# Performance work log

Measured on AMD Instinct MI355X. Metric: run time of the kernel, lower is better.

The kernel has to match this reference:

```python
import math
import jax, jax.numpy as jnp
import numpy as np

D, NH, NL, NP = 256, 8, 3, 4
HD = D // NH
SHAPES = np.array([[92, 92], [46, 46], [23, 23]], dtype=np.int32)
LSI = np.concatenate([[0], np.cumsum(SHAPES[:, 0] * SHAPES[:, 1])[:-1]]).astype(np.int32)
LV = int((SHAPES[:, 0] * SHAPES[:, 1]).sum())  # 11109
B, LQ = 2, LV


def setup_inputs() -> dict:
    key = jax.random.key(0)
    ks = jax.random.split(key, 8)
    query = jax.random.normal(ks[0], (B, LQ, D), jnp.float32)
    reference_points = jax.random.uniform(ks[1], (B, LQ, NL, 2), dtype=jnp.float32)
    value_flat = jax.random.normal(ks[2], (B, LV, D), jnp.float32)
    # sampling_offsets: small random weight + structured directional bias (as in _reset_parameters)
    W_off = jax.random.normal(ks[3], (D, NH * NL * NP * 2), jnp.float32) * 0.01
    thetas = np.arange(NH, dtype=np.float64) * (2.0 * math.pi / NH)
    g = np.stack([np.cos(thetas), np.sin(thetas)], axis=-1)
    g = g / np.abs(g).max(axis=-1, keepdims=True)
    g = np.tile(g[:, None, None, :], (1, NL, NP, 1))
    g = g * (np.arange(NP) + 1)[None, None, :, None]
    b_off = jnp.asarray(g.reshape(-1), jnp.float32)
    W_attn = jax.random.normal(ks[4], (D, NH * NL * NP), jnp.float32) * 0.01
    b_attn = jnp.zeros((NH * NL * NP,), jnp.float32)
    W_val = jax.random.normal(ks[5], (D, D), jnp.float32) * (1.0 / math.sqrt(D))
    b_val = jnp.zeros((D,), jnp.float32)
    W_out = jax.random.normal(ks[6], (D, D), jnp.float32) * (1.0 / math.sqrt(D))
    b_out = jnp.zeros((D,), jnp.float32)
    return dict(query=query, reference_points=reference_points, value_flat=value_flat,
                W_val=W_val, b_val=b_val, W_off=W_off, b_off=b_off,
                W_attn=W_attn, b_attn=b_attn, W_out=W_out, b_out=b_out,
                spatial_shapes=jnp.asarray(SHAPES), level_start_index=jnp.asarray(LSI))


def _bilinear_sample(val_l, grid):
    """torch.F.grid_sample(mode='bilinear', padding_mode='zeros', align_corners=False).
    val_l: [B,H,W,nH,hd]; grid: [B,Q,nH,P,2] with (x,y) in [-1,1].
    Returns [B,nH,Q,P,hd]."""
    Bq, H, W, nH, hd = val_l.shape
    Q, P = grid.shape[1], grid.shape[3]
    x = ((grid[..., 0] + 1.0) * W - 1.0) * 0.5   # pixel coords, align_corners=False
    y = ((grid[..., 1] + 1.0) * H - 1.0) * 0.5
    x0f, y0f = jnp.floor(x), jnp.floor(y)
    lx, ly = x - x0f, y - y0f
    x0, y0 = x0f.astype(jnp.int32), y0f.astype(jnp.int32)
    val_bh = val_l.transpose(0, 3, 1, 2, 4).reshape(Bq * nH, H * W, hd)

    def corner(yi, xi, w):
        valid = (xi >= 0) & (xi < W) & (yi >= 0) & (yi < H)
        idx = jnp.clip(yi, 0, H - 1) * W + jnp.clip(xi, 0, W - 1)   # [B,Q,nH,P]
        idx_bh = idx.transpose(0, 2, 1, 3).reshape(Bq * nH, Q * P)
        g = jnp.take_along_axis(val_bh, idx_bh[:, :, None], axis=1)  # [B*nH, Q*P, hd]
        wm = (w * valid.astype(w.dtype)).transpose(0, 2, 1, 3).reshape(Bq * nH, Q * P, 1)
        return g * wm

    out = (corner(y0, x0, (1 - ly) * (1 - lx)) + corner(y0, x0 + 1, (1 - ly) * lx)
           + corner(y0 + 1, x0, ly * (1 - lx)) + corner(y0 + 1, x0 + 1, ly * lx))
    return out.reshape(Bq, nH, Q, P, hd)


def reference(query, reference_points, value_flat, W_val, b_val, W_off, b_off,
              W_attn, b_attn, W_out, b_out, spatial_shapes, level_start_index):
    shapes = np.asarray(spatial_shapes)          # static level geometry
    starts = np.asarray(level_start_index)
    Bq, Lq, _ = query.shape
    value = (value_flat @ W_val + b_val).reshape(Bq, -1, NH, HD)
    off = (query @ W_off + b_off).reshape(Bq, Lq, NH, NL, NP, 2)        # (dy,dx) pixels
    aw = jax.nn.softmax((query @ W_attn + b_attn).reshape(Bq, Lq, NH, NL * NP), axis=-1)
    aw = aw.reshape(Bq, Lq, NH, NL, NP)
    sh_f = jnp.asarray(shapes, jnp.float32)                              # [L,2] = (H,W)
    norm_off = off / sh_f[None, None, None, :, None, :]
    loc = reference_points[:, :, None, :, None, :] + norm_off           # [B,Lq,NH,NL,NP,2] (y,x)
    grid = 2.0 * loc[..., ::-1] - 1.0                                    # (x,y) in [-1,1]
    out = jnp.zeros((Bq, Lq, NH, HD), query.dtype)
    for l in range(NL):
        H, W = int(shapes[l, 0]), int(shapes[l, 1])
        s = int(starts[l])
        val_l = value[:, s:s + H * W].reshape(Bq, H, W, NH, HD)
        sampled = _bilinear_sample(val_l, grid[:, :, :, l])              # [B,NH,Lq,NP,HD]
        out = out + jnp.einsum('bhqpc,bqhp->bqhc', sampled, aw[:, :, :, l])
    return out.reshape(Bq, Lq, D) @ W_out + b_out
```

## Files before the change

### kernel.cpp

```cpp
#include <hip/hip_runtime.h>

#define LQn   11109
#define MTOT  22218

typedef __attribute__((ext_vector_type(8))) short short8;
typedef __attribute__((ext_vector_type(4))) float f32x4;

__device__ __forceinline__ unsigned short f2bf(float f) {
  union { float f; unsigned int u; } v; v.f = f;
  unsigned int r = v.u + 0x7fffu + ((v.u >> 16) & 1u);
  return (unsigned short)(r >> 16);
}

__global__ __launch_bounds__(256) void prep_weights(
    const float* __restrict__ Wval, const float* __restrict__ Woff,
    const float* __restrict__ Wattn, const float* __restrict__ Wout,
    const float* __restrict__ boff, const float* __restrict__ battn,
    unsigned short* __restrict__ Wval_t, unsigned short* __restrict__ Wcat_t,
    unsigned short* __restrict__ Wout_t, float* __restrict__ bcat) {
  int i = blockIdx.x * 256 + threadIdx.x;
  int n = i >> 8, k = i & 255;
  if (n < 256) {
    Wval_t[i] = f2bf(Wval[k * 256 + n]);
    Wout_t[i] = f2bf(Wout[k * 256 + n]);
  }
  float src = (n < 192) ? Woff[k * 192 + n] : Wattn[k * 96 + (n - 192)];
  Wcat_t[i] = f2bf(src);
  if (i < 288) bcat[i] = (i < 192) ? boff[i] : battn[i - 192];
}

__global__ __launch_bounds__(256) void gemm_fused12(
    const float* __restrict__ Aval,
    const float* __restrict__ Aq,
    const unsigned short* __restrict__ Bval,
    const unsigned short* __restrict__ Bcat,
    const float* __restrict__ bval, const float* __restrict__ bcat,
    unsigned short* __restrict__ value16,
    float* __restrict__ logits) {
  __shared__ unsigned short As[8][64][40];
  __shared__ unsigned short Bs[64][40];

  const bool is2 = blockIdx.y == 1;
  const float* __restrict__ A = is2 ? Aq : Aval;
  const unsigned short* __restrict__ Bt = is2 ? Bcat : Bval;
  const float* __restrict__ bias = is2 ? bcat : bval;
  const int N = is2 ? 288 : 256;
  const int NB = is2 ? 5 : 4;

  const int bm = blockIdx.x;
  const int t = threadIdx.x;
  const int wave = t >> 6, lane = t & 63;
  const int wm = wave >> 1, wn = wave & 1;
  const int quad = lane >> 4, l16 = lane & 15;

  const int ldr = t >> 2;
  const int ldk = (t & 3) * 8;
  const int arow = bm * 64 + ldr;

  for (int kb = 0; kb < 8; kb++) {
    float4 a0 = {0.f, 0.f, 0.f, 0.f}, a1 = a0;
    if (arow < MTOT) {
      a0 = *(const float4*)(A + (size_t)arow * 256 + kb * 32 + ldk);
      a1 = *(const float4*)(A + (size_t)arow * 256 + kb * 32 + ldk + 4);
    }
    ushort4 lo, hi;
    lo.x = f2bf(a0.x); lo.y = f2bf(a0.y); lo.z = f2bf(a0.z); lo.w = f2bf(a0.w);
    hi.x = f2bf(a1.x); hi.y = f2bf(a1.y); hi.z = f2bf(a1.z); hi.w = f2bf(a1.w);
    *(ushort4*)(&As[kb][ldr][ldk]) = lo;
    *(ushort4*)(&As[kb][ldr][ldk + 4]) = hi;
  }

  for (int bn = 0; bn < NB; bn++) {
    const int brow = bn * 64 + ldr;
    f32x4 acc[2][2];
    for (int i = 0; i < 2; i++)
      for (int j = 0; j < 2; j++) acc[i][j] = (f32x4){0.f, 0.f, 0.f, 0.f};

    for (int kb = 0; kb < 8; kb++) {
      uint4 bv = {0u, 0u, 0u, 0u};
      if (brow < N) bv = *(const uint4*)(Bt + (size_t)brow * 256 + kb * 32 + ldk);
      __syncthreads();
      *(uint4*)(&Bs[ldr][ldk]) = bv;
      __syncthreads();
      short8 af[2], bfr[2];
      for (int i = 0; i < 2; i++)
        af[i] = *(const short8*)(&As[kb][wm * 32 + i * 16 + l16][quad * 8]);
      for (int j = 0; j < 2; j++)
        bfr[j] = *(const short8*)(&Bs[wn * 32 + j * 16 + l16][quad * 8]);
      for (int i = 0; i < 2; i++)
        for (int j = 0; j < 2; j++)
          acc[i][j] = __builtin_amdgcn_mfma_f32_16x16x32_bf16(af[i], bfr[j], acc[i][j], 0, 0, 0);
    }

    for (int i = 0; i < 2; i++)
      for (int j = 0; j < 2; j++) {
        int colg = bn * 64 + wn * 32 + j * 16 + l16;
        if (colg >= N) continue;
        float bsv = bias[colg];
        int row0 = bm * 64 + wm * 32 + i * 16 + quad * 4;
        for (int r = 0; r < 4; r++) {
          int rg = row0 + r;
          if (rg >= MTOT) continue;
          float v = acc[i][j][r] + bsv;
          if (is2) {
            logits[(size_t)rg * 288 + colg] = v;
          } else {
            int b = (rg >= LQn) ? 1 : 0;
            int p = rg - b * LQn;
            value16[((size_t)(b * 8 + (colg >> 5)) * LQn + p) * 32 + (colg & 31)] = f2bf(v);
          }
        }
      }
  }
}

__global__ __launch_bounds__(256) void gemm_a16(
    const unsigned short* __restrict__ A,
    const unsigned short* __restrict__ Bt,
    const float* __restrict__ bias,
    float* __restrict__ C) {
  __shared__ unsigned short As[8][64][40];
  __shared__ unsigned short Bs[64][40];

  const int t = threadIdx.x;
  const int bm = blockIdx.x;
  const int wave = t >> 6, lane = t & 63;
  const int wm = wave >> 1, wn = wave & 1;
  const int quad = lane >> 4, l16 = lane & 15;

  const int ldr = t >> 2;
  const int ldk = (t & 3) * 8;
  const int arow = bm * 64 + ldr;

  for (int kb = 0; kb < 8; kb++) {
    uint4 av = {0u, 0u, 0u, 0u};
    if (arow < MTOT) av = *(const uint4*)(A + (size_t)arow * 256 + kb * 32 + ldk);
    *(uint4*)(&As[kb][ldr][ldk]) = av;
  }

  for (int bn = 0; bn < 4; bn++) {
    const int brow = bn * 64 + ldr;
    f32x4 acc[2][2];
    for (int i = 0; i < 2; i++)
      for (int j = 0; j < 2; j++) acc[i][j] = (f32x4){0.f, 0.f, 0.f, 0.f};

    for (int kb = 0; kb < 8; kb++) {
      uint4 bv = *(const uint4*)(Bt + (size_t)brow * 256 + kb * 32 + ldk);
      __syncthreads();
      *(uint4*)(&Bs[ldr][ldk]) = bv;
      __syncthreads();
      short8 af[2], bfr[2];
      for (int i = 0; i < 2; i++)
        af[i] = *(const short8*)(&As[kb][wm * 32 + i * 16 + l16][quad * 8]);
      for (int j = 0; j < 2; j++)
        bfr[j] = *(const short8*)(&Bs[wn * 32 + j * 16 + l16][quad * 8]);
      for (int i = 0; i < 2; i++)
        for (int j = 0; j < 2; j++)
          acc[i][j] = __builtin_amdgcn_mfma_f32_16x16x32_bf16(af[i], bfr[j], acc[i][j], 0, 0, 0);
    }

    for (int i = 0; i < 2; i++)
      for (int j = 0; j < 2; j++) {
        int colg = bn * 64 + wn * 32 + j * 16 + l16;
        float bsv = bias[colg];
        int row0 = bm * 64 + wm * 32 + i * 16 + quad * 4;
        for (int r = 0; r < 4; r++) {
          int rg = row0 + r;
          if (rg < MTOT) C[(size_t)rg * 256 + colg] = acc[i][j][r] + bsv;
        }
      }
  }
}

__global__ __launch_bounds__(256) void msda_sample4(
    const unsigned short* __restrict__ value16,
    const float* __restrict__ logits,
    const float* __restrict__ refp,
    unsigned short* __restrict__ sampled) {
  __shared__ float          tw[8][96][4];
  __shared__ unsigned short ti[8][96][4];
  __shared__ float hmx[8][8], hrd[8][8];
  __shared__ float rfs[8][6];

  const int t = threadIdx.x;

  const int nwg = gridDim.x;
  const int xcd = blockIdx.x & 7;
  const int pos = blockIdx.x >> 3;
  const int qch = nwg >> 3, rch = nwg & 7;
  const int nbid = xcd * qch + min(xcd, rch) + pos;
  const int qbase = nbid * 8;

  if (t < 48) {
    int q = t / 6;
    if (qbase + q < MTOT) rfs[q][t - q * 6] = refp[(size_t)qbase * 6 + t];
  }
  if (t >= 64 && t < 128) {
    int tt = t - 64;
    int q = tt >> 3, h = tt & 7;
    int bq = qbase + q;
    if (bq < MTOT) {
      const float* lrow = logits + (size_t)bq * 288 + 192 + h * 12;
      float mx = -1e30f;
#pragma unroll
      for (int i = 0; i < 12; i++) mx = fmaxf(mx, lrow[i]);
      float den = 0.f;
#pragma unroll
      for (int i = 0; i < 12; i++) den += __expf(lrow[i] - mx);
      hmx[q][h] = mx;
      hrd[q][h] = 1.0f / den;
    }
  }
  __syncthreads();

  {
    const int Hs[3] = {92, 46, 23};
    const int Ss[3] = {0, 8464, 10580};
#pragma unroll
    for (int r = 0; r < 3; r++) {
      const int task = t + r * 256;
      const int q = task / 96, s = task - q * 96;
      const int bq = qbase + q;
      if (bq < MTOT) {
        const int h = s / 12, pl = s - h * 12;
        const int l = pl >> 2;
        const int H = Hs[l], W = Hs[l], S = Ss[l];
        const float* lrow = logits + (size_t)bq * 288;
        const float aw = __expf(lrow[192 + s] - hmx[q][h]) * hrd[q][h];
        const float offy = lrow[2 * s], offx = lrow[2 * s + 1];
        const float x = rfs[q][l * 2 + 1] * W + offx - 0.5f;
        const float y = rfs[q][l * 2 + 0] * H + offy - 0.5f;
        const float xf = floorf(x), yf = floorf(y);
        const int x0 = (int)xf, y0 = (int)yf;
        const float lx = x - xf, ly = y - yf;
        const bool xv0 = (x0 >= 0) & (x0 < W), xv1 = (x0 + 1 >= 0) & (x0 + 1 < W);
        const bool yv0 = (y0 >= 0) & (y0 < H), yv1 = (y0 + 1 >= 0) & (y0 + 1 < H);
        const int xc0 = min(max(x0, 0), W - 1), xc1 = min(max(x0 + 1, 0), W - 1);
        const int yc0 = min(max(y0, 0), H - 1), yc1 = min(max(y0 + 1, 0), H - 1);
        const int slot = pl * 8 + h;
        ti[q][slot][0] = (unsigned short)(S + yc0 * W + xc0);
        ti[q][slot][1] = (unsigned short)(S + yc0 * W + xc1);
        ti[q][slot][2] = (unsigned short)(S + yc1 * W + xc0);
        ti[q][slot][3] = (unsigned short)(S + yc1 * W + xc1);
        tw[q][slot][0] = (yv0 & xv0) ? aw * (1.f - ly) * (1.f - lx) : 0.f;
        tw[q][slot][1] = (yv0 & xv1) ? aw * (1.f - ly) * lx : 0.f;
        tw[q][slot][2] = (yv1 & xv0) ? aw * ly * (1.f - lx) : 0.f;
        tw[q][slot][3] = (yv1 & xv1) ? aw * ly * lx : 0.f;
      }
    }
  }
  __syncthreads();

  {
    const int w = t >> 6, lane = t & 63;
    const int q = w * 2 + (lane >> 5);
    const int h = (lane >> 2) & 7, cg = lane & 3;
    const int bq = qbase + q;
    const bool qv = bq < MTOT;
    const int bqc = qv ? bq : 0;
    const char* __restrict__ vb =
        (const char*)value16 + (size_t)(bqc / LQn) * ((size_t)LQn * 512);
    const unsigned laneoff = (unsigned)h * (LQn * 64u) + (unsigned)cg * 16u;

    float a0 = 0.f, a1 = 0.f, a2 = 0.f, a3 = 0.f;
    float a4 = 0.f, a5 = 0.f, a6 = 0.f, a7 = 0.f;
#pragma unroll
    for (int p = 0; p < 12; p++) {
      const int slot = p * 8 + h;
      const ushort4 tiv = *(const ushort4*)(&ti[q][slot][0]);
      const f32x4 wv = *(const f32x4*)(&tw[q][slot][0]);
#pragma unroll
      for (int k = 0; k < 4; k++) {
        const unsigned pix =
            (k == 0) ? tiv.x : (k == 1) ? tiv.y : (k == 2) ? tiv.z : tiv.w;
        const float wgt = wv[k];
        const uint4 u = *(const uint4*)(vb + ((pix << 6) + laneoff));
        a0 += wgt * __uint_as_float(u.x << 16);
        a1 += wgt * __uint_as_float(u.x & 0xffff0000u);
        a2 += wgt * __uint_as_float(u.y << 16);
        a3 += wgt * __uint_as_float(u.y & 0xffff0000u);
        a4 += wgt * __uint_as_float(u.z << 16);
        a5 += wgt * __uint_as_float(u.z & 0xffff0000u);
        a6 += wgt * __uint_as_float(u.w << 16);
        a7 += wgt * __uint_as_float(u.w & 0xffff0000u);
      }
    }
    if (qv) {
      uint4 o;
      o.x = (unsigned)f2bf(a0) | ((unsigned)f2bf(a1) << 16);
      o.y = (unsigned)f2bf(a2) | ((unsigned)f2bf(a3) << 16);
      o.z = (unsigned)f2bf(a4) | ((unsigned)f2bf(a5) << 16);
      o.w = (unsigned)f2bf(a6) | ((unsigned)f2bf(a7) << 16);
      *(uint4*)(sampled + (size_t)bq * 256 + h * 32 + cg * 8) = o;
    }
  }
}

extern "C" void kernel_launch(void* const* d_in, const int* in_sizes, int n_in,
                              void* d_out, int out_size, void* d_ws, size_t ws_size,
                              hipStream_t stream) {
  const float* query      = (const float*)d_in[0];
  const float* refp       = (const float*)d_in[1];
  const float* value_flat = (const float*)d_in[2];
  const float* W_val      = (const float*)d_in[3];
  const float* b_val      = (const float*)d_in[4];
  const float* W_off      = (const float*)d_in[5];
  const float* b_off      = (const float*)d_in[6];
  const float* W_attn     = (const float*)d_in[7];
  const float* b_attn     = (const float*)d_in[8];
  const float* W_out      = (const float*)d_in[9];
  const float* b_out      = (const float*)d_in[10];

  char* w = (char*)d_ws;
  size_t o = 0;
  auto carve = [&](size_t bytes) -> void* {
    void* p = (void*)(w + o);
    o += (bytes + 255) & ~(size_t)255;
    return p;
  };
  unsigned short* Wval_t  = (unsigned short*)carve(256 * 256 * 2);
  unsigned short* Wcat_t  = (unsigned short*)carve(288 * 256 * 2);
  unsigned short* Wout_t  = (unsigned short*)carve(256 * 256 * 2);
  float*          bcat    = (float*)carve(288 * 4);
  unsigned short* value16 = (unsigned short*)carve((size_t)MTOT * 256 * 2);
  float*          logits  = (float*)carve((size_t)MTOT * 288 * 4);
  unsigned short* samp_bf = (unsigned short*)carve((size_t)MTOT * 256 * 2);

  prep_weights<<<288, 256, 0, stream>>>(W_val, W_off, W_attn, W_out, b_off, b_attn,
                                        Wval_t, Wcat_t, Wout_t, bcat);

  const int mg = (MTOT + 63) / 64;
  dim3 g12(mg, 2);
  gemm_fused12<<<g12, 256, 0, stream>>>(value_flat, query, Wval_t, Wcat_t,
                                        b_val, bcat, value16, logits);

  const int sgrid = (MTOT + 7) / 8;
  msda_sample4<<<sgrid, 256, 0, stream>>>(value16, logits, refp, samp_bf);

  gemm_a16<<<mg, 256, 0, stream>>>(samp_bf, Wout_t, b_out, (float*)d_out);
}
```

Measured before the change: 195.8 us.

## Retile GEMMs to 128-row tiles with resident B and double-buffered A

Both GEMM kernels now assign one 128x64 output tile per block, with a 2D grid flattened through an XCD-aware swizzle. The full 64x256 B slice stays resident in LDS and A is double-buffered, so each k-step needs one barrier instead of two. The sampling kernel software-pipelines its gathers by prefetching the next point's four value loads before accumulating the current ones. The cost is that the fp32 A operand is re-read and re-converted by every column-tile block, where each row block previously loaded it once, and register pressure rises.

```diff
diff --git a/kernel.cpp b/kernel.cpp
--- a/kernel.cpp
+++ b/kernel.cpp
@@ -10,6 +10,21 @@
   union { float f; unsigned int u; } v; v.f = f;
   unsigned int r = v.u + 0x7fffu + ((v.u >> 16) & 1u);
   return (unsigned short)(r >> 16);
+}
+
+__device__ __forceinline__ uint4 pack8(const float4 a, const float4 b) {
+  uint4 u;
+  u.x = (unsigned)f2bf(a.x) | ((unsigned)f2bf(a.y) << 16);
+  u.y = (unsigned)f2bf(a.z) | ((unsigned)f2bf(a.w) << 16);
+  u.z = (unsigned)f2bf(b.x) | ((unsigned)f2bf(b.y) << 16);
+  u.w = (unsigned)f2bf(b.z) | ((unsigned)f2bf(b.w) << 16);
+  return u;
+}
+
+__device__ __forceinline__ int xcd_swz(int bid, int nwg) {
+  const int xcd = bid & 7, pos = bid >> 3;
+  const int q = nwg >> 3, r = nwg & 7;
+  return (xcd < r ? xcd * (q + 1) : r * (q + 1) + (xcd - r) * q) + pos;
 }
 
 __global__ __launch_bounds__(256) void prep_weights(
@@ -37,81 +52,109 @@
     const float* __restrict__ bval, const float* __restrict__ bcat,
     unsigned short* __restrict__ value16,
     float* __restrict__ logits) {
-  __shared__ unsigned short As[8][64][40];
-  __shared__ unsigned short Bs[64][40];
-
-  const bool is2 = blockIdx.y == 1;
+  __shared__ unsigned short Bs[64][264];
+  __shared__ unsigned short As[2][128][40];
+
+  const int lb = xcd_swz(blockIdx.x, gridDim.x);
+  const int bm = lb / 9;
+  const int bnid = lb - bm * 9;
+  const bool is2 = bnid >= 4;
+  const int bn = is2 ? bnid - 4 : bnid;
   const float* __restrict__ A = is2 ? Aq : Aval;
   const unsigned short* __restrict__ Bt = is2 ? Bcat : Bval;
   const float* __restrict__ bias = is2 ? bcat : bval;
   const int N = is2 ? 288 : 256;
-  const int NB = is2 ? 5 : 4;
-
-  const int bm = blockIdx.x;
+
   const int t = threadIdx.x;
   const int wave = t >> 6, lane = t & 63;
   const int wm = wave >> 1, wn = wave & 1;
   const int quad = lane >> 4, l16 = lane & 15;
 
-  const int ldr = t >> 2;
-  const int ldk = (t & 3) * 8;
-  const int arow = bm * 64 + ldr;
+  const int ar = t >> 2;
+  const int ak = (t & 3) * 8;
+
+  {
+    const int brg = bn * 64 + ar;
+    const bool bv_ok = brg < N;
+#pragma unroll
+    for (int kk = 0; kk < 8; kk++) {
+      uint4 bv = {0u, 0u, 0u, 0u};
+      if (bv_ok) bv = *(const uint4*)(Bt + (size_t)brg * 256 + kk * 32 + ak);
+      *(uint4*)(&Bs[ar][kk * 32 + ak]) = bv;
+    }
+  }
+
+  const int rg0 = bm * 128 + ar;
+  const int rg1 = rg0 + 64;
+  float4 areg[4];
+  auto loadA = [&](int kb) {
+    areg[0] = (float4){0.f, 0.f, 0.f, 0.f}; areg[1] = areg[0];
+    areg[2] = areg[0]; areg[3] = areg[0];
+    if (rg0 < MTOT) {
+      areg[0] = *(const float4*)(A + (size_t)rg0 * 256 + kb * 32 + ak);
+      areg[1] = *(const float4*)(A + (size_t)rg0 * 256 + kb * 32 + ak + 4);
+    }
+    if (rg1 < MTOT) {
+      areg[2] = *(const float4*)(A + (size_t)rg1 * 256 + kb * 32 + ak);
+      areg[3] = *(const float4*)(A + (size_t)rg1 * 256 + kb * 32 + ak + 4);
+    }
+  };
+  auto storeA = [&](int buf) {
+    *(uint4*)(&As[buf][ar][ak])      = pack8(areg[0], areg[1]);
+    *(uint4*)(&As[buf][ar + 64][ak]) = pack8(areg[2], areg[3]);
+  };
+
+  loadA(0);
+  storeA(0);
+  __syncthreads();
+
+  f32x4 acc[4][2];
+#pragma unroll
+  for (int fi = 0; fi < 4; fi++)
+#pragma unroll
+    for (int j = 0; j < 2; j++) acc[fi][j] = (f32x4){0.f, 0.f, 0.f, 0.f};
 
   for (int kb = 0; kb < 8; kb++) {
-    float4 a0 = {0.f, 0.f, 0.f, 0.f}, a1 = a0;
-    if (arow < MTOT) {
-      a0 = *(const float4*)(A + (size_t)arow * 256 + kb * 32 + ldk);
-      a1 = *(const float4*)(A + (size_t)arow * 256 + kb * 32 + ldk + 4);
-    }
-    ushort4 lo, hi;
-    lo.x = f2bf(a0.x); lo.y = f2bf(a0.y); lo.z = f2bf(a0.z); lo.w = f2bf(a0.w);
-    hi.x = f2bf(a1.x); hi.y = f2bf(a1.y); hi.z = f2bf(a1.z); hi.w = f2bf(a1.w);
-    *(ushort4*)(&As[kb][ldr][ldk]) = lo;
-    *(ushort4*)(&As[kb][ldr][ldk + 4]) = hi;
-  }
-
-  for (int bn = 0; bn < NB; bn++) {
-    const int brow = bn * 64 + ldr;
-    f32x4 acc[2][2];
-    for (int i = 0; i < 2; i++)
-      for (int j = 0; j < 2; j++) acc[i][j] = (f32x4){0.f, 0.f, 0.f, 0.f};
-
-    for (int kb = 0; kb < 8; kb++) {
-      uint4 bv = {0u, 0u, 0u, 0u};
-      if (brow < N) bv = *(const uint4*)(Bt + (size_t)brow * 256 + kb * 32 + ldk);
-      __syncthreads();
-      *(uint4*)(&Bs[ldr][ldk]) = bv;
-      __syncthreads();
-      short8 af[2], bfr[2];
-      for (int i = 0; i < 2; i++)
-        af[i] = *(const short8*)(&As[kb][wm * 32 + i * 16 + l16][quad * 8]);
+    const int cur = kb & 1;
+    if (kb < 7) loadA(kb + 1);
+    short8 af[4], bf2[2];
+#pragma unroll
+    for (int fi = 0; fi < 4; fi++)
+      af[fi] = *(const short8*)(&As[cur][wm * 64 + fi * 16 + l16][quad * 8]);
+#pragma unroll
+    for (int j = 0; j < 2; j++)
+      bf2[j] = *(const short8*)(&Bs[wn * 32 + j * 16 + l16][kb * 32 + quad * 8]);
+#pragma unroll
+    for (int fi = 0; fi < 4; fi++)
+#pragma unroll
       for (int j = 0; j < 2; j++)
-        bfr[j] = *(const short8*)(&Bs[wn * 32 + j * 16 + l16][quad * 8]);
-      for (int i = 0; i < 2; i++)
-        for (int j = 0; j < 2; j++)
-          acc[i][j] = __builtin_amdgcn_mfma_f32_16x16x32_bf16(af[i], bfr[j], acc[i][j], 0, 0, 0);
-    }
-
-    for (int i = 0; i < 2; i++)
-      for (int j = 0; j < 2; j++) {
-        int colg = bn * 64 + wn * 32 + j * 16 + l16;
-        if (colg >= N) continue;
-        float bsv = bias[colg];
-        int row0 = bm * 64 + wm * 32 + i * 16 + quad * 4;
-        for (int r = 0; r < 4; r++) {
-          int rg = row0 + r;
-          if (rg >= MTOT) continue;
-          float v = acc[i][j][r] + bsv;
-          if (is2) {
-            logits[(size_t)rg * 288 + colg] = v;
-          } else {
-            int b = (rg >= LQn) ? 1 : 0;
-            int p = rg - b * LQn;
-            value16[((size_t)(b * 8 + (colg >> 5)) * LQn + p) * 32 + (colg & 31)] = f2bf(v);
-          }
+        acc[fi][j] = __builtin_amdgcn_mfma_f32_16x16x32_bf16(af[fi], bf2[j], acc[fi][j], 0, 0, 0);
+    if (kb < 7) storeA(cur ^ 1);
+    __syncthreads();
+  }
+
+#pragma unroll
+  for (int fi = 0; fi < 4; fi++)
+#pragma unroll
+    for (int j = 0; j < 2; j++) {
+      int colg = bn * 64 + wn * 32 + j * 16 + l16;
+      if (colg >= N) continue;
+      float bsv = bias[colg];
+      int row0 = bm * 128 + wm * 64 + fi * 16 + quad * 4;
+#pragma unroll
+      for (int r = 0; r < 4; r++) {
+        int rg = row0 + r;
+        if (rg >= MTOT) continue;
+        float v = acc[fi][j][r] + bsv;
+        if (is2) {
+          logits[(size_t)rg * 288 + colg] = v;
+        } else {
+          int b = (rg >= LQn) ? 1 : 0;
+          int p = rg - b * LQn;
+          value16[((size_t)(b * 8 + (colg >> 5)) * LQn + p) * 32 + (colg & 31)] = f2bf(v);
         }
       }
-  }
+    }
 }
 
 __global__ __launch_bounds__(256) void gemm_a16(
@@ -119,57 +162,85 @@
     const unsigned short* __restrict__ Bt,
     const float* __restrict__ bias,
     float* __restrict__ C) {
-  __shared__ unsigned short As[8][64][40];
-  __shared__ unsigned short Bs[64][40];
+  __shared__ unsigned short Bs[64][264];
+  __shared__ unsigned short As[2][128][40];
+
+  const int lb = xcd_swz(blockIdx.x, gridDim.x);
+  const int bm = lb >> 2;
+  const int bn = lb & 3;
 
   const int t = threadIdx.x;
-  const int bm = blockIdx.x;
   const int wave = t >> 6, lane = t & 63;
   const int wm = wave >> 1, wn = wave & 1;
   const int quad = lane >> 4, l16 = lane & 15;
 
-  const int ldr = t >> 2;
-  const int ldk = (t & 3) * 8;
-  const int arow = bm * 64 + ldr;
+  const int ar = t >> 2;
+  const int ak = (t & 3) * 8;
+
+  {
+    const int brg = bn * 64 + ar;
+#pragma unroll
+    for (int kk = 0; kk < 8; kk++) {
+      uint4 bv = *(const uint4*)(Bt + (size_t)brg * 256 + kk * 32 + ak);
+      *(uint4*)(&Bs[ar][kk * 32 + ak]) = bv;
+    }
+  }
+
+  const int rg0 = bm * 128 + ar;
+  const int rg1 = rg0 + 64;
+  uint4 av0, av1;
+  auto loadA = [&](int kb) {
+    av0 = (uint4){0u, 0u, 0u, 0u}; av1 = av0;
+    if (rg0 < MTOT) av0 = *(const uint4*)(A + (size_t)rg0 * 256 + kb * 32 + ak);
+    if (rg1 < MTOT) av1 = *(const uint4*)(A + (size_t)rg1 * 256 + kb * 32 + ak);
+  };
+  auto storeA = [&](int buf) {
+    *(uint4*)(&As[buf][ar][ak])      = av0;
+    *(uint4*)(&As[buf][ar + 64][ak]) = av1;
+  };
+
+  loadA(0);
+  storeA(0);
+  __syncthreads();
+
+  f32x4 acc[4][2];
+#pragma unroll
+  for (int fi = 0; fi < 4; fi++)
+#pragma unroll
+    for (int j = 0; j < 2; j++) acc[fi][j] = (f32x4){0.f, 0.f, 0.f, 0.f};
 
   for (int kb = 0; kb < 8; kb++) {
-    uint4 av = {0u, 0u, 0u, 0u};
-    if (arow < MTOT) av = *(const uint4*)(A + (size_t)arow * 256 + kb * 32 + ldk);
-    *(uint4*)(&As[kb][ldr][ldk]) = av;
-  }
-
-  for (int bn = 0; bn < 4; bn++) {
-    const int brow = bn * 64 + ldr;
-    f32x4 acc[2][2];
-    for (int i = 0; i < 2; i++)
-      for (int j = 0; j < 2; j++) acc[i][j] = (f32x4){0.f, 0.f, 0.f, 0.f};
-
-    for (int kb = 0; kb < 8; kb++) {
-      uint4 bv = *(const uint4*)(Bt + (size_t)brow * 256 + kb * 32 + ldk);
-      __syncthreads();
-      *(uint4*)(&Bs[ldr][ldk]) = bv;
-      __syncthreads();
-      short8 af[2], bfr[2];
-      for (int i = 0; i < 2; i++)
-        af[i] = *(const short8*)(&As[kb][wm * 32 + i * 16 + l16][quad * 8]);
+    const int cur = kb & 1;
+    if (kb < 7) loadA(kb + 1);
+    short8 af[4], bf2[2];
+#pragma unroll
+    for (int fi = 0; fi < 4; fi++)
+      af[fi] = *(const short8*)(&As[cur][wm * 64 + fi * 16 + l16][quad * 8]);
+#pragma unroll
+    for (int j = 0; j < 2; j++)
+      bf2[j] = *(const short8*)(&Bs[wn * 32 + j * 16 + l16][kb * 32 + quad * 8]);
+#pragma unroll
+    for (int fi = 0; fi < 4; fi++)
+#pragma unroll
       for (int j = 0; j < 2; j++)
-        bfr[j] = *(const short8*)(&Bs[wn * 32 + j * 16 + l16][quad * 8]);
-      for (int i = 0; i < 2; i++)
-        for (int j = 0; j < 2; j++)
-          acc[i][j] = __builtin_amdgcn_mfma_f32_16x16x32_bf16(af[i], bfr[j], acc[i][j], 0, 0, 0);
-    }
-
-    for (int i = 0; i < 2; i++)
-      for (int j = 0; j < 2; j++) {
-        int colg = bn * 64 + wn * 32 + j * 16 + l16;
-        float bsv = bias[colg];
-        int row0 = bm * 64 + wm * 32 + i * 16 + quad * 4;
-        for (int r = 0; r < 4; r++) {
-          int rg = row0 + r;
-          if (rg < MTOT) C[(size_t)rg * 256 + colg] = acc[i][j][r] + bsv;
-        }
+        acc[fi][j] = __builtin_amdgcn_mfma_f32_16x16x32_bf16(af[fi], bf2[j], acc[fi][j], 0, 0, 0);
+    if (kb < 7) storeA(cur ^ 1);
+    __syncthreads();
+  }
+
+#pragma unroll
+  for (int fi = 0; fi < 4; fi++)
+#pragma unroll
+    for (int j = 0; j < 2; j++) {
+      int colg = bn * 64 + wn * 32 + j * 16 + l16;
+      float bsv = bias[colg];
+      int row0 = bm * 128 + wm * 64 + fi * 16 + quad * 4;
+#pragma unroll
+      for (int r = 0; r < 4; r++) {
+        int rg = row0 + r;
+        if (rg < MTOT) C[(size_t)rg * 256 + colg] = acc[fi][j][r] + bsv;
       }
-  }
+    }
 }
 
 __global__ __launch_bounds__(256) void msda_sample4(
@@ -183,12 +254,7 @@
   __shared__ float rfs[8][6];
 
   const int t = threadIdx.x;
-
-  const int nwg = gridDim.x;
-  const int xcd = blockIdx.x & 7;
-  const int pos = blockIdx.x >> 3;
-  const int qch = nwg >> 3, rch = nwg & 7;
-  const int nbid = xcd * qch + min(xcd, rch) + pos;
+  const int nbid = xcd_swz(blockIdx.x, gridDim.x);
   const int qbase = nbid * 8;
 
   if (t < 48) {
@@ -264,27 +330,44 @@
 
     float a0 = 0.f, a1 = 0.f, a2 = 0.f, a3 = 0.f;
     float a4 = 0.f, a5 = 0.f, a6 = 0.f, a7 = 0.f;
+
+#define ACC8(u, wgt)                                  \
+    a0 += (wgt) * __uint_as_float((u).x << 16);       \
+    a1 += (wgt) * __uint_as_float((u).x & 0xffff0000u); \
+    a2 += (wgt) * __uint_as_float((u).y << 16);       \
+    a3 += (wgt) * __uint_as_float((u).y & 0xffff0000u); \
+    a4 += (wgt) * __uint_as_float((u).z << 16);       \
+    a5 += (wgt) * __uint_as_float((u).z & 0xffff0000u); \
+    a6 += (wgt) * __uint_as_float((u).w << 16);       \
+    a7 += (wgt) * __uint_as_float((u).w & 0xffff0000u);
+
+    ushort4 tc = *(const ushort4*)(&ti[q][h][0]);
+    f32x4   wc = *(const f32x4*)(&tw[q][h][0]);
+    uint4 u0 = *(const uint4*)(vb + (((unsigned)tc.x << 6) + laneoff));
+    uint4 u1 = *(const uint4*)(vb + (((unsigned)tc.y << 6) + laneoff));
+    uint4 u2 = *(const uint4*)(vb + (((unsigned)tc.z << 6) + laneoff));
+    uint4 u3 = *(const uint4*)(vb + (((unsigned)tc.w << 6) + laneoff));
 #pragma unroll
     for (int p = 0; p < 12; p++) {
-      const int slot = p * 8 + h;
-      const ushort4 tiv = *(const ushort4*)(&ti[q][slot][0]);
-      const f32x4 wv = *(const f32x4*)(&tw[q][slot][0]);
-#pragma unroll
-      for (int k = 0; k < 4; k++) {
-        const unsigned pix =
-            (k == 0) ? tiv.x : (k == 1) ? tiv.y : (k == 2) ? tiv.z : tiv.w;
-        const float wgt = wv[k];
-        const uint4 u = *(const uint4*)(vb + ((pix << 6) + laneoff));
-        a0 += wgt * __uint_as_float(u.x << 16);
-        a1 += wgt * __uint_as_float(u.x & 0xffff0000u);
-        a2 += wgt * __uint_as_float(u.y << 16);
-        a3 += wgt * __uint_as_float(u.y & 0xffff0000u);
-        a4 += wgt * __uint_as_float(u.z << 16);
-        a5 += wgt * __uint_as_float(u.z & 0xffff0000u);
-        a6 += wgt * __uint_as_float(u.w << 16);
-        a7 += wgt * __uint_as_float(u.w & 0xffff0000u);
+      uint4 n0, n1, n2, n3;
+      f32x4 wn2;
+      if (p < 11) {
+        const int slot = (p + 1) * 8 + h;
+        const ushort4 tn = *(const ushort4*)(&ti[q][slot][0]);
+        wn2 = *(const f32x4*)(&tw[q][slot][0]);
+        n0 = *(const uint4*)(vb + (((unsigned)tn.x << 6) + laneoff));
+        n1 = *(const uint4*)(vb + (((unsigned)tn.y << 6) + laneoff));
+        n2 = *(const uint4*)(vb + (((unsigned)tn.z << 6) + laneoff));
+        n3 = *(const uint4*)(vb + (((unsigned)tn.w << 6) + laneoff));
       }
-    }
+      ACC8(u0, wc[0]);
+      ACC8(u1, wc[1]);
+      ACC8(u2, wc[2]);
+      ACC8(u3, wc[3]);
+      if (p < 11) { u0 = n0; u1 = n1; u2 = n2; u3 = n3; wc = wn2; }
+    }
+#undef ACC8
+
     if (qv) {
       uint4 o;
       o.x = (unsigned)f2bf(a0) | ((unsigned)f2bf(a1) << 16);
@@ -329,13 +412,12 @@
   prep_weights<<<288, 256, 0, stream>>>(W_val, W_off, W_attn, W_out, b_off, b_attn,
                                         Wval_t, Wcat_t, Wout_t, bcat);
 
-  const int mg = (MTOT + 63) / 64;
-  dim3 g12(mg, 2);
-  gemm_fused12<<<g12, 256, 0, stream>>>(value_flat, query, Wval_t, Wcat_t,
-                                        b_val, bcat, value16, logits);
+  const int mg = (MTOT + 127) / 128;
+  gemm_fused12<<<mg * 9, 256, 0, stream>>>(value_flat, query, Wval_t, Wcat_t,
+                                           b_val, bcat, value16, logits);
 
   const int sgrid = (MTOT + 7) / 8;
   msda_sample4<<<sgrid, 256, 0, stream>>>(value16, logits, refp, samp_bf);
 
-  gemm_a16<<<mg, 256, 0, stream>>>(samp_bf, Wout_t, b_out, (float*)d_out);
-}
+  gemm_a16<<<mg * 4, 256, 0, stream>>>(samp_bf, Wout_t, b_out, (float*)d_out);
+}
```

New measurement: 222.4 us. +13.6%, slower.

## Read GEMM B fragments directly from global, drop B LDS staging; prefetch sampling loads

Applied to the files above, without the earlier changes.

Both GEMM kernels now stage the whole A tile once in a padded row-major LDS buffer and load B fragments straight from global memory into registers. This removes the two barriers per k-step used for B staging. The sampling kernel software-pipelines its gathers, issuing the next point's four value loads before accumulating the current one, and the XCD swizzle is factored into a helper. The trade-off is more global traffic for B, which should mostly hit cache because B is small and shared, and higher register pressure in the sampler.

```diff
diff --git a/kernel.cpp b/kernel.cpp
--- a/kernel.cpp
+++ b/kernel.cpp
@@ -10,6 +10,21 @@
   union { float f; unsigned int u; } v; v.f = f;
   unsigned int r = v.u + 0x7fffu + ((v.u >> 16) & 1u);
   return (unsigned short)(r >> 16);
+}
+
+__device__ __forceinline__ uint4 pack8(const float4 a, const float4 b) {
+  uint4 u;
+  u.x = (unsigned)f2bf(a.x) | ((unsigned)f2bf(a.y) << 16);
+  u.y = (unsigned)f2bf(a.z) | ((unsigned)f2bf(a.w) << 16);
+  u.z = (unsigned)f2bf(b.x) | ((unsigned)f2bf(b.y) << 16);
+  u.w = (unsigned)f2bf(b.z) | ((unsigned)f2bf(b.w) << 16);
+  return u;
+}
+
+__device__ __forceinline__ int xcd_swz(int bid, int nwg) {
+  const int xcd = bid & 7, pos = bid >> 3;
+  const int q = nwg >> 3, r = nwg & 7;
+  return (xcd < r ? xcd * (q + 1) : r * (q + 1) + (xcd - r) * q) + pos;
 }
 
 __global__ __launch_bounds__(256) void prep_weights(
@@ -37,8 +52,7 @@
     const float* __restrict__ bval, const float* __restrict__ bcat,
     unsigned short* __restrict__ value16,
     float* __restrict__ logits) {
-  __shared__ unsigned short As[8][64][40];
-  __shared__ unsigned short Bs[64][40];
+  __shared__ unsigned short As[64][264];
 
   const bool is2 = blockIdx.y == 1;
   const float* __restrict__ A = is2 ? Aq : Aval;
@@ -57,47 +71,55 @@
   const int ldk = (t & 3) * 8;
   const int arow = bm * 64 + ldr;
 
+#pragma unroll
   for (int kb = 0; kb < 8; kb++) {
     float4 a0 = {0.f, 0.f, 0.f, 0.f}, a1 = a0;
     if (arow < MTOT) {
       a0 = *(const float4*)(A + (size_t)arow * 256 + kb * 32 + ldk);
       a1 = *(const float4*)(A + (size_t)arow * 256 + kb * 32 + ldk + 4);
     }
-    ushort4 lo, hi;
-    lo.x = f2bf(a0.x); lo.y = f2bf(a0.y); lo.z = f2bf(a0.z); lo.w = f2bf(a0.w);
-    hi.x = f2bf(a1.x); hi.y = f2bf(a1.y); hi.z = f2bf(a1.z); hi.w = f2bf(a1.w);
-    *(ushort4*)(&As[kb][ldr][ldk]) = lo;
-    *(ushort4*)(&As[kb][ldr][ldk + 4]) = hi;
-  }
+    *(uint4*)(&As[ldr][kb * 32 + ldk]) = pack8(a0, a1);
+  }
+  __syncthreads();
+
+  const int brow0 = wn * 32 + l16;
 
   for (int bn = 0; bn < NB; bn++) {
-    const int brow = bn * 64 + ldr;
     f32x4 acc[2][2];
+#pragma unroll
     for (int i = 0; i < 2; i++)
+#pragma unroll
       for (int j = 0; j < 2; j++) acc[i][j] = (f32x4){0.f, 0.f, 0.f, 0.f};
 
+    const int br0 = bn * 64 + brow0;
+    const int br1 = br0 + 16;
+    const unsigned short* bp0 = Bt + (size_t)br0 * 256 + quad * 8;
+    const unsigned short* bp1 = Bt + (size_t)br1 * 256 + quad * 8;
+    const bool v0 = br0 < N, v1 = br1 < N;
+
+#pragma unroll
     for (int kb = 0; kb < 8; kb++) {
-      uint4 bv = {0u, 0u, 0u, 0u};
-      if (brow < N) bv = *(const uint4*)(Bt + (size_t)brow * 256 + kb * 32 + ldk);
-      __syncthreads();
-      *(uint4*)(&Bs[ldr][ldk]) = bv;
-      __syncthreads();
       short8 af[2], bfr[2];
+      af[0] = *(const short8*)(&As[wm * 32 + l16][kb * 32 + quad * 8]);
+      af[1] = *(const short8*)(&As[wm * 32 + 16 + l16][kb * 32 + quad * 8]);
+      bfr[0] = v0 ? *(const short8*)(bp0 + kb * 32) : (short8){0,0,0,0,0,0,0,0};
+      bfr[1] = v1 ? *(const short8*)(bp1 + kb * 32) : (short8){0,0,0,0,0,0,0,0};
+#pragma unroll
       for (int i = 0; i < 2; i++)
-        af[i] = *(const short8*)(&As[kb][wm * 32 + i * 16 + l16][quad * 8]);
-      for (int j = 0; j < 2; j++)
-        bfr[j] = *(const short8*)(&Bs[wn * 32 + j * 16 + l16][quad * 8]);
-      for (int i = 0; i < 2; i++)
+#pragma unroll
         for (int j = 0; j < 2; j++)
           acc[i][j] = __builtin_amdgcn_mfma_f32_16x16x32_bf16(af[i], bfr[j], acc[i][j], 0, 0, 0);
     }
 
+#pragma unroll
     for (int i = 0; i < 2; i++)
+#pragma unroll
       for (int j = 0; j < 2; j++) {
         int colg = bn * 64 + wn * 32 + j * 16 + l16;
         if (colg >= N) continue;
         float bsv = bias[colg];
         int row0 = bm * 64 + wm * 32 + i * 16 + quad * 4;
+#pragma unroll
         for (int r = 0; r < 4; r++) {
           int rg = row0 + r;
           if (rg >= MTOT) continue;
@@ -119,11 +141,10 @@
     const unsigned short* __restrict__ Bt,
     const float* __restrict__ bias,
     float* __restrict__ C) {
-  __shared__ unsigned short As[8][64][40];
-  __shared__ unsigned short Bs[64][40];
-
+  __shared__ unsigned short As[64][264];
+
+  const int bm = blockIdx.x;
   const int t = threadIdx.x;
-  const int bm = blockIdx.x;
   const int wave = t >> 6, lane = t & 63;
   const int wm = wave >> 1, wn = wave & 1;
   const int quad = lane >> 4, l16 = lane & 15;
@@ -132,38 +153,49 @@
   const int ldk = (t & 3) * 8;
   const int arow = bm * 64 + ldr;
 
+#pragma unroll
   for (int kb = 0; kb < 8; kb++) {
     uint4 av = {0u, 0u, 0u, 0u};
     if (arow < MTOT) av = *(const uint4*)(A + (size_t)arow * 256 + kb * 32 + ldk);
-    *(uint4*)(&As[kb][ldr][ldk]) = av;
-  }
+    *(uint4*)(&As[ldr][kb * 32 + ldk]) = av;
+  }
+  __syncthreads();
+
+  const int brow0 = wn * 32 + l16;
 
   for (int bn = 0; bn < 4; bn++) {
-    const int brow = bn * 64 + ldr;
     f32x4 acc[2][2];
+#pragma unroll
     for (int i = 0; i < 2; i++)
+#pragma unroll
       for (int j = 0; j < 2; j++) acc[i][j] = (f32x4){0.f, 0.f, 0.f, 0.f};
 
+    const int br0 = bn * 64 + brow0;
+    const unsigned short* bp0 = Bt + (size_t)br0 * 256 + quad * 8;
+    const unsigned short* bp1 = bp0 + 16 * 256;
+
+#pragma unroll
     for (int kb = 0; kb < 8; kb++) {
-      uint4 bv = *(const uint4*)(Bt + (size_t)brow * 256 + kb * 32 + ldk);
-      __syncthreads();
-      *(uint4*)(&Bs[ldr][ldk]) = bv;
-      __syncthreads();
       short8 af[2], bfr[2];
+      af[0] = *(const short8*)(&As[wm * 32 + l16][kb * 32 + quad * 8]);
+      af[1] = *(const short8*)(&As[wm * 32 + 16 + l16][kb * 32 + quad * 8]);
+      bfr[0] = *(const short8*)(bp0 + kb * 32);
+      bfr[1] = *(const short8*)(bp1 + kb * 32);
+#pragma unroll
       for (int i = 0; i < 2; i++)
-        af[i] = *(const short8*)(&As[kb][wm * 32 + i * 16 + l16][quad * 8]);
-      for (int j = 0; j < 2; j++)
-        bfr[j] = *(const short8*)(&Bs[wn * 32 + j * 16 + l16][quad * 8]);
-      for (int i = 0; i < 2; i++)
+#pragma unroll
         for (int j = 0; j < 2; j++)
           acc[i][j] = __builtin_amdgcn_mfma_f32_16x16x32_bf16(af[i], bfr[j], acc[i][j], 0, 0, 0);
     }
 
+#pragma unroll
     for (int i = 0; i < 2; i++)
+#pragma unroll
       for (int j = 0; j < 2; j++) {
         int colg = bn * 64 + wn * 32 + j * 16 + l16;
         float bsv = bias[colg];
         int row0 = bm * 64 + wm * 32 + i * 16 + quad * 4;
+#pragma unroll
         for (int r = 0; r < 4; r++) {
           int rg = row0 + r;
           if (rg < MTOT) C[(size_t)rg * 256 + colg] = acc[i][j][r] + bsv;
@@ -183,12 +215,7 @@
   __shared__ float rfs[8][6];
 
   const int t = threadIdx.x;
-
-  const int nwg = gridDim.x;
-  const int xcd = blockIdx.x & 7;
-  const int pos = blockIdx.x >> 3;
-  const int qch = nwg >> 3, rch = nwg & 7;
-  const int nbid = xcd * qch + min(xcd, rch) + pos;
+  const int nbid = xcd_swz(blockIdx.x, gridDim.x);
   const int qbase = nbid * 8;
 
   if (t < 48) {
@@ -264,27 +291,44 @@
 
     float a0 = 0.f, a1 = 0.f, a2 = 0.f, a3 = 0.f;
     float a4 = 0.f, a5 = 0.f, a6 = 0.f, a7 = 0.f;
+
+#define ACC8(u, wgt)                                  \
+    a0 += (wgt) * __uint_as_float((u).x << 16);       \
+    a1 += (wgt) * __uint_as_float((u).x & 0xffff0000u); \
+    a2 += (wgt) * __uint_as_float((u).y << 16);       \
+    a3 += (wgt) * __uint_as_float((u).y & 0xffff0000u); \
+    a4 += (wgt) * __uint_as_float((u).z << 16);       \
+    a5 += (wgt) * __uint_as_float((u).z & 0xffff0000u); \
+    a6 += (wgt) * __uint_as_float((u).w << 16);       \
+    a7 += (wgt) * __uint_as_float((u).w & 0xffff0000u);
+
+    ushort4 tc = *(const ushort4*)(&ti[q][h][0]);
+    f32x4   wc = *(const f32x4*)(&tw[q][h][0]);
+    uint4 u0 = *(const uint4*)(vb + (((unsigned)tc.x << 6) + laneoff));
+    uint4 u1 = *(const uint4*)(vb + (((unsigned)tc.y << 6) + laneoff));
+    uint4 u2 = *(const uint4*)(vb + (((unsigned)tc.z << 6) + laneoff));
+    uint4 u3 = *(const uint4*)(vb + (((unsigned)tc.w << 6) + laneoff));
 #pragma unroll
     for (int p = 0; p < 12; p++) {
-      const int slot = p * 8 + h;
-      const ushort4 tiv = *(const ushort4*)(&ti[q][slot][0]);
-      const f32x4 wv = *(const f32x4*)(&tw[q][slot][0]);
-#pragma unroll
-      for (int k = 0; k < 4; k++) {
-        const unsigned pix =
-            (k == 0) ? tiv.x : (k == 1) ? tiv.y : (k == 2) ? tiv.z : tiv.w;
-        const float wgt = wv[k];
-        const uint4 u = *(const uint4*)(vb + ((pix << 6) + laneoff));
-        a0 += wgt * __uint_as_float(u.x << 16);
-        a1 += wgt * __uint_as_float(u.x & 0xffff0000u);
-        a2 += wgt * __uint_as_float(u.y << 16);
-        a3 += wgt * __uint_as_float(u.y & 0xffff0000u);
-        a4 += wgt * __uint_as_float(u.z << 16);
-        a5 += wgt * __uint_as_float(u.z & 0xffff0000u);
-        a6 += wgt * __uint_as_float(u.w << 16);
-        a7 += wgt * __uint_as_float(u.w & 0xffff0000u);
+      uint4 n0, n1, n2, n3;
+      f32x4 wn2;
+      if (p < 11) {
+        const int slot = (p + 1) * 8 + h;
+        const ushort4 tn = *(const ushort4*)(&ti[q][slot][0]);
+        wn2 = *(const f32x4*)(&tw[q][slot][0]);
+        n0 = *(const uint4*)(vb + (((unsigned)tn.x << 6) + laneoff));
+        n1 = *(const uint4*)(vb + (((unsigned)tn.y << 6) + laneoff));
+        n2 = *(const uint4*)(vb + (((unsigned)tn.z << 6) + laneoff));
+        n3 = *(const uint4*)(vb + (((unsigned)tn.w << 6) + laneoff));
       }
-    }
+      ACC8(u0, wc[0]);
+      ACC8(u1, wc[1]);
+      ACC8(u2, wc[2]);
+      ACC8(u3, wc[3]);
+      if (p < 11) { u0 = n0; u1 = n1; u2 = n2; u3 = n3; wc = wn2; }
+    }
+#undef ACC8
+
     if (qv) {
       uint4 o;
       o.x = (unsigned)f2bf(a0) | ((unsigned)f2bf(a1) << 16);
```

After: 214.7 us. 1.1x slower.

## Stage full-K B tile in LDS and keep A fragments in registers in GEMMs

Applied to the files above, without the earlier changes.

Both GEMM kernels now load the whole 64x256 B tile into shared memory once per column block instead of once per 32-wide K step. This cuts the barriers per column block from sixteen to two. A fragments are read from LDS once into registers and reused across all column blocks, and fp32-to-bf16 packing is vectorized. The cost is a larger LDS footprint (about 67KB per block), which may limit occupancy, plus more register pressure from holding 16 A fragments. The XCD swizzle is refactored into a helper function.

```diff
diff --git a/kernel.cpp b/kernel.cpp
--- a/kernel.cpp
+++ b/kernel.cpp
@@ -10,6 +10,21 @@
   union { float f; unsigned int u; } v; v.f = f;
   unsigned int r = v.u + 0x7fffu + ((v.u >> 16) & 1u);
   return (unsigned short)(r >> 16);
+}
+
+__device__ __forceinline__ uint4 pack8(const float4 a, const float4 b) {
+  uint4 u;
+  u.x = (unsigned)f2bf(a.x) | ((unsigned)f2bf(a.y) << 16);
+  u.y = (unsigned)f2bf(a.z) | ((unsigned)f2bf(a.w) << 16);
+  u.z = (unsigned)f2bf(b.x) | ((unsigned)f2bf(b.y) << 16);
+  u.w = (unsigned)f2bf(b.z) | ((unsigned)f2bf(b.w) << 16);
+  return u;
+}
+
+__device__ __forceinline__ int xcd_swz(int bid, int nwg) {
+  const int xcd = bid & 7, pos = bid >> 3;
+  const int q = nwg >> 3, r = nwg & 7;
+  return (xcd < r ? xcd * (q + 1) : r * (q + 1) + (xcd - r) * q) + pos;
 }
 
 __global__ __launch_bounds__(256) void prep_weights(
@@ -37,8 +52,8 @@
     const float* __restrict__ bval, const float* __restrict__ bcat,
     unsigned short* __restrict__ value16,
     float* __restrict__ logits) {
-  __shared__ unsigned short As[8][64][40];
-  __shared__ unsigned short Bs[64][40];
+  __shared__ unsigned short As[64][264];
+  __shared__ unsigned short Bs[64][264];
 
   const bool is2 = blockIdx.y == 1;
   const float* __restrict__ A = is2 ? Aq : Aval;
@@ -57,56 +72,82 @@
   const int ldk = (t & 3) * 8;
   const int arow = bm * 64 + ldr;
 
+#pragma unroll
   for (int kb = 0; kb < 8; kb++) {
     float4 a0 = {0.f, 0.f, 0.f, 0.f}, a1 = a0;
     if (arow < MTOT) {
       a0 = *(const float4*)(A + (size_t)arow * 256 + kb * 32 + ldk);
       a1 = *(const float4*)(A + (size_t)arow * 256 + kb * 32 + ldk + 4);
     }
-    ushort4 lo, hi;
-    lo.x = f2bf(a0.x); lo.y = f2bf(a0.y); lo.z = f2bf(a0.z); lo.w = f2bf(a0.w);
-    hi.x = f2bf(a1.x); hi.y = f2bf(a1.y); hi.z = f2bf(a1.z); hi.w = f2bf(a1.w);
-    *(ushort4*)(&As[kb][ldr][ldk]) = lo;
-    *(ushort4*)(&As[kb][ldr][ldk + 4]) = hi;
-  }
+    *(uint4*)(&As[ldr][kb * 32 + ldk]) = pack8(a0, a1);
+  }
+  __syncthreads();
+
+  short8 af[8][2];
+#pragma unroll
+  for (int kb = 0; kb < 8; kb++) {
+    af[kb][0] = *(const short8*)(&As[wm * 32 + l16][kb * 32 + quad * 8]);
+    af[kb][1] = *(const short8*)(&As[wm * 32 + 16 + l16][kb * 32 + quad * 8]);
+  }
+
+  const int bcol = (t & 3) * 64;
 
   for (int bn = 0; bn < NB; bn++) {
-    const int brow = bn * 64 + ldr;
+    __syncthreads();
+    {
+      const int brg = bn * 64 + ldr;
+      const bool ok = brg < N;
+#pragma unroll
+      for (int u = 0; u < 4; u++) {
+        uint4 b0 = {0u, 0u, 0u, 0u};
+        if (ok) b0 = *(const uint4*)(Bt + (size_t)brg * 256 + bcol + u * 8);
+        *(uint4*)(&Bs[ldr][bcol + u * 8]) = b0;
+      }
+#pragma unroll
+      for (int u = 4; u < 8; u++) {
+        uint4 b0 = {0u, 0u, 0u, 0u};
+        if (ok) b0 = *(const uint4*)(Bt + (size_t)brg * 256 + bcol + u * 8);
+        *(uint4*)(&Bs[ldr][bcol + u * 8]) = b0;
+      }
+    }
+    __syncthreads();
+
     f32x4 acc[2][2];
+#pragma unroll
     for (int i = 0; i < 2; i++)
+#pragma unroll
       for (int j = 0; j < 2; j++) acc[i][j] = (f32x4){0.f, 0.f, 0.f, 0.f};
 
+#pragma unroll
     for (int kb = 0; kb < 8; kb++) {
-      uint4 bv = {0u, 0u, 0u, 0u};
-      if (brow < N) bv = *(const uint4*)(Bt + (size_t)brow * 256 + kb * 32 + ldk);
-      __syncthreads();
-      *(uint4*)(&Bs[ldr][ldk]) = bv;
-      __syncthreads();
-      short8 af[2], bfr[2];
+      short8 bfr[2];
+      bfr[0] = *(const short8*)(&Bs[wn * 32 + l16][kb * 32 + quad * 8]);
+      bfr[1] = *(const short8*)(&Bs[wn * 32 + 16 + l16][kb * 32 + quad * 8]);
+#pragma unroll
       for (int i = 0; i < 2; i++)
-        af[i] = *(const short8*)(&As[kb][wm * 32 + i * 16 + l16][quad * 8]);
-      for (int j = 0; j < 2; j++)
-        bfr[j] = *(const short8*)(&Bs[wn * 32 + j * 16 + l16][quad * 8]);
-      for (int i = 0; i < 2; i++)
+#pragma unroll
         for (int j = 0; j < 2; j++)
-          acc[i][j] = __builtin_amdgcn_mfma_f32_16x16x32_bf16(af[i], bfr[j], acc[i][j], 0, 0, 0);
-    }
-
+          acc[i][j] = __builtin_amdgcn_mfma_f32_16x16x32_bf16(af[kb][i], bfr[j], acc[i][j], 0, 0, 0);
+    }
+
+#pragma unroll
     for (int i = 0; i < 2; i++)
+#pragma unroll
       for (int j = 0; j < 2; j++) {
-        int colg = bn * 64 + wn * 32 + j * 16 + l16;
+        const int colg = bn * 64 + wn * 32 + j * 16 + l16;
         if (colg >= N) continue;
-        float bsv = bias[colg];
-        int row0 = bm * 64 + wm * 32 + i * 16 + quad * 4;
+        const float bsv = bias[colg];
+        const int row0 = bm * 64 + wm * 32 + i * 16 + quad * 4;
+#pragma unroll
         for (int r = 0; r < 4; r++) {
-          int rg = row0 + r;
+          const int rg = row0 + r;
           if (rg >= MTOT) continue;
-          float v = acc[i][j][r] + bsv;
+          const float v = acc[i][j][r] + bsv;
           if (is2) {
             logits[(size_t)rg * 288 + colg] = v;
           } else {
-            int b = (rg >= LQn) ? 1 : 0;
-            int p = rg - b * LQn;
+            const int b = (rg >= LQn) ? 1 : 0;
+            const int p = rg - b * LQn;
             value16[((size_t)(b * 8 + (colg >> 5)) * LQn + p) * 32 + (colg & 31)] = f2bf(v);
           }
         }
@@ -119,11 +160,11 @@
     const unsigned short* __restrict__ Bt,
     const float* __restrict__ bias,
     float* __restrict__ C) {
-  __shared__ unsigned short As[8][64][40];
-  __shared__ unsigned short Bs[64][40];
-
+  __shared__ unsigned short As[64][264];
+  __shared__ unsigned short Bs[64][264];
+
+  const int bm = blockIdx.x;
   const int t = threadIdx.x;
-  const int bm = blockIdx.x;
   const int wave = t >> 6, lane = t & 63;
   const int wm = wave >> 1, wn = wave & 1;
   const int quad = lane >> 4, l16 = lane & 15;
@@ -132,40 +173,63 @@
   const int ldk = (t & 3) * 8;
   const int arow = bm * 64 + ldr;
 
+#pragma unroll
   for (int kb = 0; kb < 8; kb++) {
     uint4 av = {0u, 0u, 0u, 0u};
     if (arow < MTOT) av = *(const uint4*)(A + (size_t)arow * 256 + kb * 32 + ldk);
-    *(uint4*)(&As[kb][ldr][ldk]) = av;
-  }
+    *(uint4*)(&As[ldr][kb * 32 + ldk]) = av;
+  }
+  __syncthreads();
+
+  short8 af[8][2];
+#pragma unroll
+  for (int kb = 0; kb < 8; kb++) {
+    af[kb][0] = *(const short8*)(&As[wm * 32 + l16][kb * 32 + quad * 8]);
+    af[kb][1] = *(const short8*)(&As[wm * 32 + 16 + l16][kb * 32 + quad * 8]);
+  }
+
+  const int bcol = (t & 3) * 64;
 
   for (int bn = 0; bn < 4; bn++) {
-    const int brow = bn * 64 + ldr;
+    __syncthreads();
+    {
+      const int brg = bn * 64 + ldr;
+#pragma unroll
+      for (int u = 0; u < 8; u++) {
+        uint4 b0 = *(const uint4*)(Bt + (size_t)brg * 256 + bcol + u * 8);
+        *(uint4*)(&Bs[ldr][bcol + u * 8]) = b0;
+      }
+    }
+    __syncthreads();
+
     f32x4 acc[2][2];
+#pragma unroll
     for (int i = 0; i < 2; i++)
+#pragma unroll
       for (int j = 0; j < 2; j++) acc[i][j] = (f32x4){0.f, 0.f, 0.f, 0.f};
 
+#pragma unroll
     for (int kb = 0; kb < 8; kb++) {
-      uint4 bv = *(const uint4*)(Bt + (size_t)brow * 256 + kb * 32 + ldk);
-      __syncthreads();
-      *(uint4*)(&Bs[ldr][ldk]) = bv;
-      __syncthreads();
-      short8 af[2], bfr[2];
+      short8 bfr[2];
+      bfr[0] = *(const short8*)(&Bs[wn * 32 + l16][kb * 32 + quad * 8]);
+      bfr[1] = *(const short8*)(&Bs[wn * 32 + 16 + l16][kb * 32 + quad * 8]);
+#pragma unroll
       for (int i = 0; i < 2; i++)
-        af[i] = *(const short8*)(&As[kb][wm * 32 + i * 16 + l16][quad * 8]);
-      for (int j = 0; j < 2; j++)
-        bfr[j] = *(const short8*)(&Bs[wn * 32 + j * 16 + l16][quad * 8]);
-      for (int i = 0; i < 2; i++)
+#pragma unroll
         for (int j = 0; j < 2; j++)
-          acc[i][j] = __builtin_amdgcn_mfma_f32_16x16x32_bf16(af[i], bfr[j], acc[i][j], 0, 0, 0);
-    }
-
+          acc[i][j] = __builtin_amdgcn_mfma_f32_16x16x32_bf16(af[kb][i], bfr[j], acc[i][j], 0, 0, 0);
+    }
+
+#pragma unroll
     for (int i = 0; i < 2; i++)
+#pragma unroll
       for (int j = 0; j < 2; j++) {
-        int colg = bn * 64 + wn * 32 + j * 16 + l16;
-        float bsv = bias[colg];
-        int row0 = bm * 64 + wm * 32 + i * 16 + quad * 4;
+        const int colg = bn * 64 + wn * 32 + j * 16 + l16;
+        const float bsv = bias[colg];
+        const int row0 = bm * 64 + wm * 32 + i * 16 + quad * 4;
+#pragma unroll
         for (int r = 0; r < 4; r++) {
-          int rg = row0 + r;
+          const int rg = row0 + r;
           if (rg < MTOT) C[(size_t)rg * 256 + colg] = acc[i][j][r] + bsv;
         }
       }
@@ -183,12 +247,7 @@
   __shared__ float rfs[8][6];
 
   const int t = threadIdx.x;
-
-  const int nwg = gridDim.x;
-  const int xcd = blockIdx.x & 7;
-  const int pos = blockIdx.x >> 3;
-  const int qch = nwg >> 3, rch = nwg & 7;
-  const int nbid = xcd * qch + min(xcd, rch) + pos;
+  const int nbid = xcd_swz(blockIdx.x, gridDim.x);
   const int qbase = nbid * 8;
 
   if (t < 48) {
```

Result: slower. 212.0 us (+8.3%).
